# Kernel optimization log

Measured on AMD Instinct MI355X. Metric: run time of the kernel, lower is better.

The kernel has to match this reference:

```python
import jax, jax.numpy as jnp
import numpy as np

EPS = 1e-5

def _layer_norm(x, gamma, beta):
    mu = jnp.mean(x, axis=-1, keepdims=True)
    var = jnp.mean(jnp.square(x - mu), axis=-1, keepdims=True)
    return (x - mu) * jax.lax.rsqrt(var + EPS) * gamma + beta

def setup_inputs() -> dict:
    key = jax.random.key(0)
    ks = jax.random.split(key, 4)
    B, S, D, F = 4, 2048, 1024, 4096
    return {
        "hidden_state": jax.random.normal(ks[0], (B, S, D), dtype=jnp.float32),
        "attention_mask": jnp.zeros((B, S), dtype=jnp.float32),
        "w1": jax.random.normal(ks[1], (D, F), dtype=jnp.float32) * (1.0 / np.sqrt(D)),
        "b1": jnp.zeros((F,), dtype=jnp.float32),
        "w2": jax.random.normal(ks[2], (F, D), dtype=jnp.float32) * (1.0 / np.sqrt(F)),
        "b2": jnp.zeros((D,), dtype=jnp.float32),
        "ln1_gamma": jnp.ones((D,), dtype=jnp.float32),
        "ln1_beta": jnp.zeros((D,), dtype=jnp.float32),
        "ln2_gamma": jnp.ones((D,), dtype=jnp.float32),
        "ln2_beta": jnp.zeros((D,), dtype=jnp.float32),
    }

def reference(hidden_state, attention_mask, w1, b1, w2, b2,
              ln1_gamma, ln1_beta, ln2_gamma, ln2_beta):
    h = hidden_state
    d = h.shape[-1]
    # Self-attention with Q=K=V=h (no projections), single head.
    scores = jnp.einsum("bqd,bkd->bqk", h, h) / jnp.sqrt(jnp.float32(d))
    scores = scores + attention_mask[:, None, :]  # additive mask [B,1,S]
    probs = jax.nn.softmax(scores, axis=-1)
    attn_out = jnp.einsum("bqk,bkd->bqd", probs, h)
    # Residual + post-LN (dropout inactive in eval)
    h = _layer_norm(h + attn_out, ln1_gamma, ln1_beta)
    # FFN: Linear -> exact GELU -> Linear
    ffn = jax.nn.gelu(h @ w1 + b1, approximate=False) @ w2 + b2
    h = _layer_norm(h + ffn, ln2_gamma, ln2_beta)
    return h
```

## Files before the change

kernel.cpp:

```cpp
#include <hip/hip_runtime.h>
#include <hip/hip_bf16.h>
#include <math.h>

typedef __bf16 bf16;
typedef __bf16 bf16x8 __attribute__((ext_vector_type(8)));
typedef float  f32x4  __attribute__((ext_vector_type(4)));

__device__ __forceinline__ float gelu_f(float x) {
    return 0.5f * x * (1.0f + erff(x * 0.70710678118654752440f));
}

__global__ void detect_k(const unsigned short* __restrict__ h, int* __restrict__ flag)
{
    if (threadIdx.x == 0 && blockIdx.x == 0) {
        int cnt = 0;
        for (int i = 0; i < 256; i += 2) {
            int e = (h[i] >> 7) & 0xFF;
            cnt += (e >= 100 && e <= 140) ? 1 : 0;
        }
        *flag = (cnt >= 96) ? 0 : 1;
    }
}

struct SmallConvArgs {
    const void* src[7];
    bf16* dst[7];
    int n[7];
};
__global__ __launch_bounds__(256) void small_convert_k(SmallConvArgs a,
                                                       const int* __restrict__ flag)
{
    const int seg = blockIdx.y;
    const int i = blockIdx.x * 256 + threadIdx.x;
    if (i >= a.n[seg]) return;
    const float v = (*flag) ? ((const float*)a.src[seg])[i]
                            : (float)((const bf16*)a.src[seg])[i];
    a.dst[seg][i] = (bf16)v;
}

__global__ __launch_bounds__(256) void conv_transpose_k(
    const void* __restrict__ in, bf16* __restrict__ outT,
    int R, int C, const int* __restrict__ flag)
{
    __shared__ bf16 tile[32][33];
    const int c0 = blockIdx.x * 32;
    const int r0 = blockIdx.y * 32;
    const int tx = threadIdx.x & 31;
    const int ty = threadIdx.x >> 5;
    const bool f32 = (*flag) != 0;
#pragma unroll
    for (int i = 0; i < 32; i += 8) {
        const long idx = (long)(r0 + ty + i) * C + (c0 + tx);
        const float v = f32 ? ((const float*)in)[idx] : (float)((const bf16*)in)[idx];
        tile[ty + i][tx] = (bf16)v;
    }
    __syncthreads();
#pragma unroll
    for (int i = 0; i < 32; i += 8)
        outT[(long)(c0 + ty + i) * R + (r0 + tx)] = tile[tx][ty + i];
}

__global__ __launch_bounds__(256) void conv_transpose_h_k(
    const void* __restrict__ in, bf16* __restrict__ h_bf, bf16* __restrict__ hT,
    int S, int D, const int* __restrict__ flag)
{
    __shared__ bf16 tile[32][33];
    const long sB = (long)S * D;
    const int d0 = blockIdx.x * 32;
    const int s0 = blockIdx.y * 32;
    const int b  = blockIdx.z;
    const int tx = threadIdx.x & 31;
    const int ty = threadIdx.x >> 5;
    const bool f32 = (*flag) != 0;
#pragma unroll
    for (int i = 0; i < 32; i += 8) {
        const long idx = b * sB + (long)(s0 + ty + i) * D + (d0 + tx);
        const float v = f32 ? ((const float*)in)[idx] : (float)((const bf16*)in)[idx];
        const bf16 bv = (bf16)v;
        h_bf[idx] = bv;
        tile[ty + i][tx] = bv;
    }
    __syncthreads();
#pragma unroll
    for (int i = 0; i < 32; i += 8)
        hT[b * sB + (long)(d0 + ty + i) * S + (s0 + tx)] = tile[tx][ty + i];
}

__device__ __forceinline__ void gll16(const bf16* g, bf16* l)
{
    __builtin_amdgcn_global_load_lds(
        (const __attribute__((address_space(1))) void*)g,
        (__attribute__((address_space(3))) void*)l, 16, 0, 0);
}

template <int MODE, int STAGE>
__global__ __launch_bounds__(256) void gemm_nt(
    const bf16* __restrict__ A, const bf16* __restrict__ Bt,
    bf16* __restrict__ C, const bf16* __restrict__ bias,
    int M, int N, int K, float scale,
    long sA, long sB, long sC)
{
    A  += (long)blockIdx.z * sA;
    Bt += (long)blockIdx.z * sB;
    C  += (long)blockIdx.z * sC;

    const int tileM = blockIdx.y * 128;
    const int tileN = blockIdx.x * 128;

    __shared__ __align__(16) bf16 As[128 * 64];
    __shared__ __align__(16) bf16 Bs[128 * 64];

    const int t    = threadIdx.x;
    const int lane = t & 63;
    const int wave = t >> 6;
    const int wr   = wave >> 1;
    const int wc   = wave & 1;
    const int quad = lane >> 4;
    const int l16  = lane & 15;

    const int srow   = lane >> 3;
    const int lchunk = ((lane & 7) - srow) & 7;

    f32x4 acc[4][4] = {};

    auto swz = [](int row, int chunk) { return row * 64 + (((chunk + row) & 7) * 8); };

    for (int k0 = 0; k0 < K; k0 += 64) {
        if constexpr (STAGE == 1) {
#pragma unroll
            for (int r2 = 0; r2 < 4; ++r2) {
                const int unit = wave * 4 + r2;
                const int row  = unit * 8 + srow;
                const int col  = lchunk * 8;
                gll16(A  + (long)(tileM + row) * K + (k0 + col), As + unit * 512);
                gll16(Bt + (long)(tileN + row) * K + (k0 + col), Bs + unit * 512);
            }
            __syncthreads();
        } else {
            bf16x8 ra[4], rb[4];
#pragma unroll
            for (int r = 0; r < 4; ++r) {
                const int e   = (r * 256 + t) * 8;
                const int row = e >> 6;
                const int col = e & 63;
                ra[r] = *(const bf16x8*)(A  + (long)(tileM + row) * K + (k0 + col));
                rb[r] = *(const bf16x8*)(Bt + (long)(tileN + row) * K + (k0 + col));
            }
#pragma unroll
            for (int r = 0; r < 4; ++r) {
                const int row = (r * 256 + t) >> 3;
                const int off = swz(row, t & 7);
                *(bf16x8*)&As[off] = ra[r];
                *(bf16x8*)&Bs[off] = rb[r];
            }
            __syncthreads();
        }

#pragma unroll
        for (int kk = 0; kk < 64; kk += 32) {
            const int chunk = (kk >> 3) + quad;
            bf16x8 af[4], bfr[4];
#pragma unroll
            for (int i = 0; i < 4; ++i) {
                af[i]  = *(const bf16x8*)&As[swz(wr * 64 + i * 16 + l16, chunk)];
                bfr[i] = *(const bf16x8*)&Bs[swz(wc * 64 + i * 16 + l16, chunk)];
            }
#pragma unroll
            for (int mi = 0; mi < 4; ++mi)
#pragma unroll
                for (int ni = 0; ni < 4; ++ni)
                    acc[mi][ni] = __builtin_amdgcn_mfma_f32_16x16x32_bf16(
                        af[mi], bfr[ni], acc[mi][ni], 0, 0, 0);
        }
        __syncthreads();
    }

#pragma unroll
    for (int mi = 0; mi < 4; ++mi) {
        const int rbase = tileM + wr * 64 + mi * 16 + quad * 4;
#pragma unroll
        for (int ni = 0; ni < 4; ++ni) {
            const int col = tileN + wc * 64 + ni * 16 + l16;
            float bv = 0.0f;
            if (MODE >= 2) bv = (float)bias[col];
#pragma unroll
            for (int r = 0; r < 4; ++r) {
                float v = acc[mi][ni][r];
                if (MODE == 0) v *= scale;
                if (MODE >= 2) v += bv;
                if (MODE == 2) v = gelu_f(v);
                C[(long)(rbase + r) * N + col] = (bf16)v;
            }
        }
    }
}

__global__ __launch_bounds__(256) void softmax_k(
    bf16* __restrict__ scores, const bf16* __restrict__ mask, int S)
{
    const long rowOff = ((long)blockIdx.y * S + blockIdx.x) * S;
    bf16* row = scores + rowOff;
    const bf16* mrow = mask + (long)blockIdx.y * S;
    const int t = threadIdx.x;

    const bf16x8 r = ((const bf16x8*)row)[t];
    const bf16x8 m = ((const bf16x8*)mrow)[t];
    float v[8];
    float mx = -1e30f;
#pragma unroll
    for (int i = 0; i < 8; ++i) {
        v[i] = (float)r[i] + (float)m[i];
        mx = fmaxf(mx, v[i]);
    }
#pragma unroll
    for (int off = 32; off > 0; off >>= 1)
        mx = fmaxf(mx, __shfl_down(mx, off));
    __shared__ float redm[4];
    if ((t & 63) == 0) redm[t >> 6] = mx;
    __syncthreads();
    mx = fmaxf(fmaxf(redm[0], redm[1]), fmaxf(redm[2], redm[3]));

    float s = 0.0f;
#pragma unroll
    for (int i = 0; i < 8; ++i) { v[i] = __expf(v[i] - mx); s += v[i]; }
#pragma unroll
    for (int off = 32; off > 0; off >>= 1)
        s += __shfl_down(s, off);
    __shared__ float reds[4];
    if ((t & 63) == 0) reds[t >> 6] = s;
    __syncthreads();
    s = reds[0] + reds[1] + reds[2] + reds[3];
    const float inv = 1.0f / s;
    bf16x8 o;
#pragma unroll
    for (int i = 0; i < 8; ++i) o[i] = (bf16)(v[i] * inv);
    ((bf16x8*)row)[t] = o;
}

__global__ __launch_bounds__(128) void ln_residual_k(
    const bf16* __restrict__ x1, const bf16* __restrict__ x2,
    const bf16* __restrict__ gamma, const bf16* __restrict__ beta,
    bf16* __restrict__ out)
{
    constexpr int D = 1024;
    const long off = (long)blockIdx.x * D;
    const int t = threadIdx.x;
    const bf16x8 a = ((const bf16x8*)(x1 + off))[t];
    const bf16x8 b = ((const bf16x8*)(x2 + off))[t];
    float v[8];
    float s = 0.0f, s2 = 0.0f;
#pragma unroll
    for (int i = 0; i < 8; ++i) {
        v[i] = (float)a[i] + (float)b[i];
        s  += v[i];
        s2 += v[i] * v[i];
    }
#pragma unroll
    for (int o2 = 32; o2 > 0; o2 >>= 1) {
        s  += __shfl_down(s, o2);
        s2 += __shfl_down(s2, o2);
    }
    __shared__ float rs[2], rs2[2];
    if ((t & 63) == 0) { rs[t >> 6] = s; rs2[t >> 6] = s2; }
    __syncthreads();
    s  = rs[0] + rs[1];
    s2 = rs2[0] + rs2[1];
    const float mean = s / (float)D;
    const float var  = s2 / (float)D - mean * mean;
    const float inv  = rsqrtf(var + 1e-5f);
    const bf16x8 g  = ((const bf16x8*)gamma)[t];
    const bf16x8 be = ((const bf16x8*)beta)[t];
    bf16x8 o;
#pragma unroll
    for (int i = 0; i < 8; ++i)
        o[i] = (bf16)((v[i] - mean) * inv * (float)g[i] + (float)be[i]);
    ((bf16x8*)(out + off))[t] = o;
}

__global__ __launch_bounds__(128) void ln_out_k(
    const bf16* __restrict__ x1, const bf16* __restrict__ x2,
    const bf16* __restrict__ gamma, const bf16* __restrict__ beta,
    void* __restrict__ outv, const int* __restrict__ flag)
{
    constexpr int D = 1024;
    const long off = (long)blockIdx.x * D;
    const int t = threadIdx.x;
    const bf16x8 a = ((const bf16x8*)(x1 + off))[t];
    const bf16x8 b = ((const bf16x8*)(x2 + off))[t];
    float v[8];
    float s = 0.0f, s2 = 0.0f;
#pragma unroll
    for (int i = 0; i < 8; ++i) {
        v[i] = (float)a[i] + (float)b[i];
        s  += v[i];
        s2 += v[i] * v[i];
    }
#pragma unroll
    for (int o2 = 32; o2 > 0; o2 >>= 1) {
        s  += __shfl_down(s, o2);
        s2 += __shfl_down(s2, o2);
    }
    __shared__ float rs[2], rs2[2];
    if ((t & 63) == 0) { rs[t >> 6] = s; rs2[t >> 6] = s2; }
    __syncthreads();
    s  = rs[0] + rs[1];
    s2 = rs2[0] + rs2[1];
    const float mean = s / (float)D;
    const float var  = s2 / (float)D - mean * mean;
    const float inv  = rsqrtf(var + 1e-5f);
    const bf16x8 g  = ((const bf16x8*)gamma)[t];
    const bf16x8 be = ((const bf16x8*)beta)[t];
    if (*flag) {
        f32x4 o1, o2v;
#pragma unroll
        for (int i = 0; i < 4; ++i) {
            o1[i]  = (v[i] - mean) * inv * (float)g[i] + (float)be[i];
            o2v[i] = (v[4 + i] - mean) * inv * (float)g[4 + i] + (float)be[4 + i];
        }
        f32x4* op = (f32x4*)((float*)outv + off);
        op[t * 2]     = o1;
        op[t * 2 + 1] = o2v;
    } else {
        bf16x8 o;
#pragma unroll
        for (int i = 0; i < 8; ++i)
            o[i] = (bf16)((v[i] - mean) * inv * (float)g[i] + (float)be[i]);
        ((bf16x8*)((bf16*)outv + off))[t] = o;
    }
}

extern "C" void kernel_launch(void* const* d_in, const int* in_sizes, int n_in,
                              void* d_out, int out_size, void* d_ws, size_t ws_size,
                              hipStream_t stream)
{
    constexpr int B = 4, S = 2048, D = 1024, F = 4096;
    constexpr long MB = 1024 * 1024;

    const void* h_raw  = d_in[0];
    const void* mk_raw = d_in[1];
    const void* w1_raw = d_in[2];
    const void* b1_raw = d_in[3];
    const void* w2_raw = d_in[4];
    const void* b2_raw = d_in[5];
    const void* g1_raw = d_in[6];
    const void* be1_raw= d_in[7];
    const void* g2_raw = d_in[8];
    const void* be2_raw= d_in[9];

    char* ws = (char*)d_ws;
    bf16* scores = (bf16*)(ws + 0);
    bf16* gact   = (bf16*)(ws + 0);
    bf16* hT     = (bf16*)(ws + 32 * MB);
    bf16* h_bf   = (bf16*)(ws + 48 * MB);
    bf16* y1     = (bf16*)(ws + 64 * MB);
    bf16* w1T    = (bf16*)(ws + 80 * MB);
    bf16* w2T    = (bf16*)(ws + 88 * MB);
    bf16* axf    = (bf16*)(ws + 96 * MB);
    char* sm     = ws + 112 * MB;
    int*  flag   = (int*)(sm);
    bf16* mk_bf  = (bf16*)(sm + 1024);
    bf16* b1_bf  = (bf16*)(sm + 17408 + 1024);
    bf16* b2_bf  = (bf16*)(sm + 25600 + 3072);
    bf16* g1_bf  = (bf16*)(sm + 27648 + 3072);
    bf16* be1_bf = (bf16*)(sm + 29696 + 3072);
    bf16* g2_bf  = (bf16*)(sm + 31744 + 3072);
    bf16* be2_bf = (bf16*)(sm + 33792 + 3072);

    const long SD = (long)S * D;
    const long SS = (long)S * S;

    detect_k<<<1, 64, 0, stream>>>((const unsigned short*)h_raw, flag);

    SmallConvArgs sca;
    sca.src[0] = mk_raw;  sca.dst[0] = mk_bf;  sca.n[0] = B * S;
    sca.src[1] = b1_raw;  sca.dst[1] = b1_bf;  sca.n[1] = F;
    sca.src[2] = b2_raw;  sca.dst[2] = b2_bf;  sca.n[2] = D;
    sca.src[3] = g1_raw;  sca.dst[3] = g1_bf;  sca.n[3] = D;
    sca.src[4] = be1_raw; sca.dst[4] = be1_bf; sca.n[4] = D;
    sca.src[5] = g2_raw;  sca.dst[5] = g2_bf;  sca.n[5] = D;
    sca.src[6] = be2_raw; sca.dst[6] = be2_bf; sca.n[6] = D;
    small_convert_k<<<dim3((B * S) / 256, 7), 256, 0, stream>>>(sca, flag);

    conv_transpose_h_k<<<dim3(D / 32, S / 32, B), 256, 0, stream>>>(
        h_raw, h_bf, hT, S, D, flag);

    conv_transpose_k<<<dim3(F / 32, D / 32), 256, 0, stream>>>(w1_raw, w1T, D, F, flag);
    conv_transpose_k<<<dim3(D / 32, F / 32), 256, 0, stream>>>(w2_raw, w2T, F, D, flag);

    gemm_nt<0, 1><<<dim3(S / 128, S / 128, B), 256, 0, stream>>>(
        h_bf, h_bf, scores, nullptr, S, S, D, 0.03125f, SD, SD, SS);

    softmax_k<<<dim3(S, B), 256, 0, stream>>>(scores, mk_bf, S);

    gemm_nt<1, 0><<<dim3(D / 128, S / 128, B), 256, 0, stream>>>(
        scores, hT, axf, nullptr, S, D, S, 1.0f, SS, SD, SD);

    ln_residual_k<<<B * S, 128, 0, stream>>>(h_bf, axf, g1_bf, be1_bf, y1);

    gemm_nt<2, 1><<<dim3(F / 128, (B * S) / 128, 1), 256, 0, stream>>>(
        y1, w1T, gact, b1_bf, B * S, F, D, 1.0f, 0, 0, 0);

    gemm_nt<3, 1><<<dim3(D / 128, (B * S) / 128, 1), 256, 0, stream>>>(
        gact, w2T, axf, b2_bf, B * S, D, F, 1.0f, 0, 0, 0);

    ln_out_k<<<B * S, 128, 0, stream>>>(y1, axf, g2_bf, be2_bf, d_out, flag);
}
```

Baseline: 491.8 us.

## Double-buffer LDS in GEMM with async global-to-LDS prefetch

Adds a STAGE==2 path to the bf16 MFMA GEMM that ping-pongs between two LDS buffers, so the async global-to-LDS load of the next K tile is issued before computing the current one. This lets memory latency overlap with MFMA work and removes one barrier per K step. It doubles LDS use per block to 64KB, which can lower occupancy. The P·V GEMM also moves from the register-staged load path to the direct global-to-LDS path.

```diff
diff --git a/kernel.cpp b/kernel.cpp
--- a/kernel.cpp
+++ b/kernel.cpp
@@ -107,9 +107,6 @@
     const int tileM = blockIdx.y * 128;
     const int tileN = blockIdx.x * 128;
 
-    __shared__ __align__(16) bf16 As[128 * 64];
-    __shared__ __align__(16) bf16 Bs[128 * 64];
-
     const int t    = threadIdx.x;
     const int lane = t & 63;
     const int wave = t >> 6;
@@ -125,45 +122,26 @@
 
     auto swz = [](int row, int chunk) { return row * 64 + (((chunk + row) & 7) * 8); };
 
-    for (int k0 = 0; k0 < K; k0 += 64) {
-        if constexpr (STAGE == 1) {
-#pragma unroll
-            for (int r2 = 0; r2 < 4; ++r2) {
-                const int unit = wave * 4 + r2;
-                const int row  = unit * 8 + srow;
-                const int col  = lchunk * 8;
-                gll16(A  + (long)(tileM + row) * K + (k0 + col), As + unit * 512);
-                gll16(Bt + (long)(tileN + row) * K + (k0 + col), Bs + unit * 512);
-            }
-            __syncthreads();
-        } else {
-            bf16x8 ra[4], rb[4];
-#pragma unroll
-            for (int r = 0; r < 4; ++r) {
-                const int e   = (r * 256 + t) * 8;
-                const int row = e >> 6;
-                const int col = e & 63;
-                ra[r] = *(const bf16x8*)(A  + (long)(tileM + row) * K + (k0 + col));
-                rb[r] = *(const bf16x8*)(Bt + (long)(tileN + row) * K + (k0 + col));
-            }
-#pragma unroll
-            for (int r = 0; r < 4; ++r) {
-                const int row = (r * 256 + t) >> 3;
-                const int off = swz(row, t & 7);
-                *(bf16x8*)&As[off] = ra[r];
-                *(bf16x8*)&Bs[off] = rb[r];
-            }
-            __syncthreads();
-        }
-
+    auto stage = [&](bf16* as, bf16* bs, int k0) {
+#pragma unroll
+        for (int r2 = 0; r2 < 4; ++r2) {
+            const int unit = wave * 4 + r2;
+            const int row  = unit * 8 + srow;
+            const int col  = lchunk * 8;
+            gll16(A  + (long)(tileM + row) * K + (k0 + col), as + unit * 512);
+            gll16(Bt + (long)(tileN + row) * K + (k0 + col), bs + unit * 512);
+        }
+    };
+
+    auto compute = [&](const bf16* as, const bf16* bs) {
 #pragma unroll
         for (int kk = 0; kk < 64; kk += 32) {
             const int chunk = (kk >> 3) + quad;
             bf16x8 af[4], bfr[4];
 #pragma unroll
             for (int i = 0; i < 4; ++i) {
-                af[i]  = *(const bf16x8*)&As[swz(wr * 64 + i * 16 + l16, chunk)];
-                bfr[i] = *(const bf16x8*)&Bs[swz(wc * 64 + i * 16 + l16, chunk)];
+                af[i]  = *(const bf16x8*)&as[swz(wr * 64 + i * 16 + l16, chunk)];
+                bfr[i] = *(const bf16x8*)&bs[swz(wc * 64 + i * 16 + l16, chunk)];
             }
 #pragma unroll
             for (int mi = 0; mi < 4; ++mi)
@@ -172,7 +150,37 @@
                     acc[mi][ni] = __builtin_amdgcn_mfma_f32_16x16x32_bf16(
                         af[mi], bfr[ni], acc[mi][ni], 0, 0, 0);
         }
+    };
+
+    if constexpr (STAGE == 2) {
+        __shared__ __align__(16) bf16 As0[128 * 64];
+        __shared__ __align__(16) bf16 As1[128 * 64];
+        __shared__ __align__(16) bf16 Bs0[128 * 64];
+        __shared__ __align__(16) bf16 Bs1[128 * 64];
+
+        stage(As0, Bs0, 0);
         __syncthreads();
+        for (int u = 0; u < K / 64; u += 2) {
+            const int k1 = (u + 1) * 64;
+            const int k2 = (u + 2) * 64;
+            if (k1 < K) stage(As1, Bs1, k1);
+            compute(As0, Bs0);
+            __syncthreads();
+            if (k1 < K) {
+                if (k2 < K) stage(As0, Bs0, k2);
+                compute(As1, Bs1);
+                __syncthreads();
+            }
+        }
+    } else {
+        __shared__ __align__(16) bf16 As[128 * 64];
+        __shared__ __align__(16) bf16 Bs[128 * 64];
+        for (int k0 = 0; k0 < K; k0 += 64) {
+            stage(As, Bs, k0);
+            __syncthreads();
+            compute(As, Bs);
+            __syncthreads();
+        }
     }
 
 #pragma unroll
@@ -387,20 +395,20 @@
     conv_transpose_k<<<dim3(F / 32, D / 32), 256, 0, stream>>>(w1_raw, w1T, D, F, flag);
     conv_transpose_k<<<dim3(D / 32, F / 32), 256, 0, stream>>>(w2_raw, w2T, F, D, flag);
 
-    gemm_nt<0, 1><<<dim3(S / 128, S / 128, B), 256, 0, stream>>>(
+    gemm_nt<0, 2><<<dim3(S / 128, S / 128, B), 256, 0, stream>>>(
         h_bf, h_bf, scores, nullptr, S, S, D, 0.03125f, SD, SD, SS);
 
     softmax_k<<<dim3(S, B), 256, 0, stream>>>(scores, mk_bf, S);
 
-    gemm_nt<1, 0><<<dim3(D / 128, S / 128, B), 256, 0, stream>>>(
+    gemm_nt<1, 1><<<dim3(D / 128, S / 128, B), 256, 0, stream>>>(
         scores, hT, axf, nullptr, S, D, S, 1.0f, SS, SD, SD);
 
     ln_residual_k<<<B * S, 128, 0, stream>>>(h_bf, axf, g1_bf, be1_bf, y1);
 
-    gemm_nt<2, 1><<<dim3(F / 128, (B * S) / 128, 1), 256, 0, stream>>>(
+    gemm_nt<2, 2><<<dim3(F / 128, (B * S) / 128, 1), 256, 0, stream>>>(
         y1, w1T, gact, b1_bf, B * S, F, D, 1.0f, 0, 0, 0);
 
-    gemm_nt<3, 1><<<dim3(D / 128, (B * S) / 128, 1), 256, 0, stream>>>(
+    gemm_nt<3, 2><<<dim3(D / 128, (B * S) / 128, 1), 256, 0, stream>>>(
         gact, w2T, axf, b2_bf, B * S, D, F, 1.0f, 0, 0, 0);
 
     ln_out_k<<<B * S, 128, 0, stream>>>(y1, axf, g2_bf, be2_bf, d_out, flag);
```

Measured after the change: 450.4 us. 8.4% less time.
